# Kernel optimization log

Measured on AMD Instinct MI355X. Metric: run time of the kernel, lower is better.

The kernel has to match this reference:

```python
import jax, jax.numpy as jnp
import numpy as np
from jax.scipy.special import logsumexp

K, V, D, R, S_ITERS = 512, 50257, 300, 75, 20


def setup_inputs() -> dict:
    key = jax.random.key(0)
    ks = jax.random.split(key, 4)
    word_embeds = jax.random.normal(ks[0], (V, D), dtype=jnp.float32)  # frozen GloVe table
    anchors = jax.random.normal(ks[1], (K, D), dtype=jnp.float32) * 0.02
    M_U = jax.random.normal(ks[2], (D, R), dtype=jnp.float32) * (1.0 / D ** 0.5)
    # word_proj initialized to identity in torch (nn.init.eye_); add tiny noise to avoid degeneracy
    Wp = jnp.eye(D, dtype=jnp.float32) + 0.01 * jax.random.normal(ks[3], (D, D), dtype=jnp.float32)
    log_eps = jnp.float32(-2.3)
    topic_scale = jnp.ones((K, 1), dtype=jnp.float32)
    return {"word_embeds": word_embeds, "anchors": anchors, "M_U": M_U,
            "Wp": Wp, "log_eps": log_eps, "topic_scale": topic_scale}


def _l2norm(x):
    # F.normalize(dim=-1) with eps clamp
    n = jnp.maximum(jnp.linalg.norm(x, axis=-1, keepdims=True), 1e-12)
    return x / n


def reference(word_embeds, anchors, M_U, Wp, log_eps, topic_scale):
    # torch Linear: x @ W.T
    w = _l2norm(word_embeds @ Wp.T)   # [V, d]
    a = _l2norm(anchors)              # [K, d]

    # Mahalanobis cost with M = I + U U^T
    M = jnp.eye(D, dtype=w.dtype) + M_U @ M_U.T    # [d, d]
    MA = a @ M                                      # [K, d]
    MW = w @ M                                      # [V, d]
    AA = jnp.sum(MA * a, axis=-1)                   # [K]
    WW = jnp.sum(MW * w, axis=-1)                   # [V]
    cost = jnp.maximum(AA[:, None] + WW[None, :] - 2.0 * (MA @ w.T), 0.0)  # [K, V]

    eps = jax.nn.softplus(log_eps) + 1e-4
    log_kern = -cost / eps                          # [K, V]

    # 20-step log-domain Sinkhorn
    def body(carry, _):
        log_u, log_v = carry
        log_u = -logsumexp(log_kern + log_v, axis=1, keepdims=True)  # [K, 1]
        log_v = -logsumexp(log_kern + log_u, axis=0, keepdims=True)  # [1, V]
        return (log_u, log_v), None

    init = (jnp.zeros((K, 1), log_kern.dtype), jnp.zeros((1, V), log_kern.dtype))
    (log_u, log_v), _ = jax.lax.scan(body, init, None, length=S_ITERS)

    log_P = log_kern + log_u + log_v
    log_beta = log_P - logsumexp(log_P, axis=1, keepdims=True)
    beta = jnp.exp(log_beta) * jax.nn.softplus(topic_scale)
    beta = beta / jnp.sum(beta, axis=1, keepdims=True)
    return beta  # [K, V]
```

## Files before the change

### kernel.cpp

```cpp
#include <hip/hip_runtime.h>
#include <math.h>

#define KT 512
#define VW 50257
#define DD 300
#define RR 75
#define DR 375
#define GAMMA 0.010187536f
#define NB 786
#define SLOTS 8

typedef _Float16 half8 __attribute__((ext_vector_type(8)));
typedef float f32x4 __attribute__((ext_vector_type(4)));

__device__ __forceinline__ void load_lds16(const void* g, void* l) {
  __builtin_amdgcn_global_load_lds(
      (const __attribute__((address_space(1))) unsigned int*)g,
      (__attribute__((address_space(3))) unsigned int*)l, 16, 0, 0);
}

__device__ inline float block_reduce_sum(float val, float* sbuf) {
  int t = threadIdx.x;
  sbuf[t] = val;
  __syncthreads();
  for (int off = blockDim.x >> 1; off > 0; off >>= 1) {
    if (t < off) sbuf[t] += sbuf[t + off];
    __syncthreads();
  }
  float r = sbuf[0];
  __syncthreads();
  return r;
}

template <int CTRL>
__device__ __forceinline__ float dpp_add_step(float x) {
  int yi = __builtin_amdgcn_update_dpp(0, __float_as_int(x), CTRL, 0xf, 0xf, false);
  return x + __int_as_float(yi);
}
__device__ __forceinline__ float wave_reduce_add(float x) {
  x = dpp_add_step<0x111>(x);
  x = dpp_add_step<0x112>(x);
  x = dpp_add_step<0x114>(x);
  x = dpp_add_step<0x118>(x);
  x = dpp_add_step<0x142>(x);
  x = dpp_add_step<0x143>(x);
  return x;
}

__global__ void prep_We_split(const float* __restrict__ We, _Float16* __restrict__ We2) {
  int v = blockIdx.x, c = threadIdx.x;
  float x = (c < DD) ? We[(size_t)v * DD + c] : 0.f;
  _Float16 h = (_Float16)x;
  We2[(size_t)v * 640 + c] = h;
  We2[(size_t)v * 640 + 320 + c] = (_Float16)(x - (float)h);
}

__global__ void prep_bext(const float* __restrict__ Wp, const float* __restrict__ MU,
                          float* __restrict__ Bext) {
  int id = blockIdx.x * blockDim.x + threadIdx.x;
  if (id >= DR * DD) return;
  int row = id / DD, d = id - row * DD;
  if (row < DD) {
    Bext[id] = Wp[row * DD + d];
  } else {
    int r = row - DD;
    float s = 0.f;
    for (int j = 0; j < DD; ++j) s += MU[j * RR + r] * Wp[j * DD + d];
    Bext[id] = s;
  }
}

__global__ void prep_bext_split(const float* __restrict__ BextR, _Float16* __restrict__ Bext2) {
  int r = blockIdx.x, c = threadIdx.x;
  float x = (r < DR && c < DD) ? BextR[r * DD + c] : 0.f;
  _Float16 h = (_Float16)x;
  Bext2[(size_t)r * 640 + c] = h;
  Bext2[(size_t)r * 640 + 320 + c] = (_Float16)(x - (float)h);
}

__global__ void prep_anchors(const float* __restrict__ anchors, const float* __restrict__ MU,
                             _Float16* __restrict__ Ahat2, float* __restrict__ AA) {
  __shared__ float a[DD];
  __shared__ float psh[RR];
  __shared__ float red[128];
  __shared__ float inv_sh;
  int k = blockIdx.x, t = threadIdx.x;
  float ss = 0.f;
  for (int d = t; d < DD; d += 128) {
    float x = anchors[k * DD + d];
    a[d] = x;
    ss += x * x;
  }
  ss = block_reduce_sum(ss, red);
  if (t == 0) inv_sh = 1.f / fmaxf(sqrtf(ss), 1e-12f);
  __syncthreads();
  float inv = inv_sh;
  float p2 = 0.f;
  if (t < RR) {
    float p = 0.f;
    for (int j = 0; j < DD; ++j) p += MU[j * RR + t] * a[j];
    p *= inv;
    psh[t] = p;
    p2 = p * p;
  }
  p2 = block_reduce_sum(p2, red);
  _Float16* row = Ahat2 + (size_t)k * 768;
  for (int d = t; d < 384; d += 128) {
    float val = (d < DD) ? a[d] * inv : ((d < DR) ? psh[d - DD] : 0.f);
    _Float16 h = (_Float16)val;
    row[d] = h;
    row[384 + d] = (_Float16)(val - (float)h);
  }
  if (t == 0) AA[k] = 1.f + p2;
}

__global__ void prep_words(float* __restrict__ WhatR, float* __restrict__ WW) {
  __shared__ float red[128];
  __shared__ float inv_sh;
  int v = blockIdx.x, t = threadIdx.x;
  float* rowf = WhatR + (size_t)v * 384;
  float x0 = rowf[t];
  float x1 = rowf[t + 128];
  float x2 = (t + 256 < DR) ? rowf[t + 256] : 0.f;
  float ss = x0 * x0 + x1 * x1 + ((t < 44) ? x2 * x2 : 0.f);
  ss = block_reduce_sum(ss, red);
  if (t == 0) inv_sh = 1.f / fmaxf(sqrtf(ss), 1e-12f);
  __syncthreads();
  float inv = inv_sh;
  x0 *= inv; x1 *= inv; x2 *= inv;
  float p2 = (t >= 44 && t + 256 < DR) ? x2 * x2 : 0.f;
  p2 = block_reduce_sum(p2, red);
  _Float16* rowh = (_Float16*)rowf;
  _Float16 h0 = (_Float16)x0;
  rowh[t] = h0; rowh[384 + t] = (_Float16)(x0 - (float)h0);
  _Float16 h1 = (_Float16)x1;
  rowh[128 + t] = h1; rowh[512 + t] = (_Float16)(x1 - (float)h1);
  float v2 = (t + 256 < DR) ? x2 : 0.f;
  _Float16 h2 = (_Float16)v2;
  rowh[256 + t] = h2; rowh[640 + t] = (_Float16)(v2 - (float)h2);
  if (t == 0) WW[v] = 1.f + p2;
}

template <int EPI>
__global__ __launch_bounds__(256) void gemm_mfma(
    const _Float16* __restrict__ Ag, int ldaE,
    const _Float16* __restrict__ Bg, int ldbE,
    float* __restrict__ C, long ldc,
    int M, int N, int KTOT, int SEGL, int mOnX,
    const float* __restrict__ AAv, const float* __restrict__ WWv,
    const float* __restrict__ log_eps_ptr) {
  __shared__ __align__(16) _Float16 As[128 * 64];
  __shared__ __align__(16) _Float16 Bs[128 * 64];
  int t = threadIdx.x, lane = t & 63, w = t >> 6;

  int nwg = gridDim.x * gridDim.y;
  int orig = blockIdx.y * gridDim.x + blockIdx.x;
  int q = nwg >> 3, r8 = nwg & 7;
  int xcd = orig & 7, pos = orig >> 3;
  int wgid = (xcd < r8 ? xcd * (q + 1) : r8 * (q + 1) + (xcd - r8) * q) + pos;
  int bxi = wgid % gridDim.x;
  int byi = wgid / gridDim.x;

  int bm = (mOnX ? bxi : byi) * 128;
  int bn = (mOnX ? byi : bxi) * 128;
  int wm = w >> 1, wn = w & 1;
  f32x4 acc[4][4] = {};
  size_t ldaB = (size_t)ldaE * 2, ldbB = (size_t)ldbE * 2;
  int srow = lane >> 3, sg = lane & 7;
  int lr = lane & 15, kq = lane >> 4;

  for (int k0 = 0; k0 < KTOT; k0 += 64) {
    int ak = (k0 >= 2 * SEGL) ? k0 - 2 * SEGL : k0;
    int bk = (k0 >= SEGL) ? k0 - SEGL : k0;
    size_t akb = (size_t)ak * 2, bkb = (size_t)bk * 2;
#pragma unroll
    for (int qq = 0; qq < 4; ++qq) {
      int iid = w * 4 + qq;
      int r = iid * 8 + srow;
      int gs = sg ^ (r & 7);
      int gmr = bm + r; if (gmr >= M) gmr = M - 1;
      load_lds16((const char*)Ag + (size_t)gmr * ldaB + akb + (gs << 4),
                 (char*)As + iid * 1024);
      int gnr = bn + r; if (gnr >= N) gnr = N - 1;
      load_lds16((const char*)Bg + (size_t)gnr * ldbB + bkb + (gs << 4),
                 (char*)Bs + iid * 1024);
    }
    __syncthreads();
#pragma unroll
    for (int ks = 0; ks < 2; ++ks) {
      half8 af[4], bf[4];
#pragma unroll
      for (int i = 0; i < 4; ++i) {
        int row = wm * 64 + i * 16 + lr;
        af[i] = *(const half8*)((const char*)As + row * 128 +
                                ((((ks << 2) + kq) ^ (row & 7)) << 4));
        int col = wn * 64 + i * 16 + lr;
        bf[i] = *(const half8*)((const char*)Bs + col * 128 +
                                ((((ks << 2) + kq) ^ (col & 7)) << 4));
      }
#pragma unroll
      for (int i = 0; i < 4; ++i)
#pragma unroll
        for (int j = 0; j < 4; ++j)
          acc[i][j] = __builtin_amdgcn_mfma_f32_16x16x32_f16(af[i], bf[j], acc[i][j], 0, 0, 0);
    }
    __syncthreads();
  }

  float s2e = 0.f;
  if (EPI == 1) {
    float le = log_eps_ptr[0];
    float eps = log1pf(__expf(le)) + 1e-4f;
    s2e = 1.4426950408889634f / eps;
  }
  int rq = lane >> 4;
#pragma unroll
  for (int i = 0; i < 4; ++i) {
#pragma unroll
    for (int j = 0; j < 4; ++j) {
#pragma unroll
      for (int r = 0; r < 4; ++r) {
        int gm = bm + wm * 64 + i * 16 + rq * 4 + r;
        int gn = bn + wn * 64 + j * 16 + lr;
        if (gm < M && gn < N) {
          float c = acc[i][j][r];
          if (EPI == 0) {
            C[(size_t)gm * ldc + gn] = c;
          } else {
            float e = exp2f((2.f * c - AAv[gm] - WWv[gn]) * s2e);
            C[(size_t)gm * ldc + gn] = fminf(e, 1.0f);
          }
        }
      }
    }
  }
}

template <int FIRST>
__global__ __launch_bounds__(512) void sweep(const float* __restrict__ E,
                                             const float* __restrict__ Sprev,
                                             float* __restrict__ Scur,
                                             float* __restrict__ vout) {
  __shared__ float u_sh[KT];
  __shared__ float colp[8][64];
  __shared__ float v_sh[64];
  __shared__ float rowacc[KT];
  int t = threadIdx.x;
  int c1 = t & 63, kr = t >> 6;
  int c0 = blockIdx.x * 64;
  int col = c0 + c1;
  bool valid = col < VW;

  if (!FIRST) {
    float s = 0.f;
#pragma unroll
    for (int q = 0; q < SLOTS; ++q) s += Sprev[q * KT + t];
    u_sh[t] = 1.0f / fmaxf(s, 1e-35f);
    __syncthreads();
  }

  float tile[64];
  const float* p = E + (size_t)kr * VW + col;
#pragma unroll
  for (int j = 0; j < 64; ++j) {
    tile[j] = valid ? *p : 0.f;
    p += (size_t)8 * VW;
  }

  float v;
  if (FIRST) {
    v = 1.0f;
  } else {
    float cs = 0.f;
#pragma unroll
    for (int j = 0; j < 64; ++j) cs = fmaf(tile[j], u_sh[kr + 8 * j], cs);
    colp[kr][c1] = cs;
    __syncthreads();
    if (t < 64) {
      float s = 0.f;
#pragma unroll
      for (int q = 0; q < 8; ++q) s += colp[q][t];
      float vv = (c0 + t < VW) ? GAMMA / fmaxf(s, 1e-35f) : 0.f;
      v_sh[t] = vv;
      if (c0 + t < VW) vout[c0 + t] = vv;
    }
    __syncthreads();
    v = v_sh[c1];
  }

#pragma unroll
  for (int j = 0; j < 64; ++j) {
    float x = wave_reduce_add(tile[j] * v);
    if (c1 == 63) rowacc[kr + 8 * j] = x;
  }
  __syncthreads();
  unsafeAtomicAdd(&Scur[(blockIdx.x & (SLOTS - 1)) * KT + t], rowacc[t]);
}

__global__ __launch_bounds__(256) void write_beta(float* __restrict__ out,
                                                  const float* __restrict__ Sfin,
                                                  const float* __restrict__ vv) {
  __shared__ float uk_sh;
  int k = blockIdx.y;
  int t = threadIdx.x;
  if (t == 0) {
    float s = 0.f;
#pragma unroll
    for (int q = 0; q < SLOTS; ++q) s += Sfin[q * KT + k];
    uk_sh = 1.0f / fmaxf(s, 1e-35f);
  }
  __syncthreads();
  float uk = uk_sh;
  int v = blockIdx.x * 256 + t;
  if (v >= VW) return;
  size_t id = (size_t)k * VW + v;
  out[id] = out[id] * (uk * vv[v]);
}

extern "C" void kernel_launch(void* const* d_in, const int* in_sizes, int n_in,
                              void* d_out, int out_size, void* d_ws, size_t ws_size,
                              hipStream_t stream) {
  const float* We = (const float*)d_in[0];
  const float* An = (const float*)d_in[1];
  const float* MU = (const float*)d_in[2];
  const float* Wp = (const float*)d_in[3];
  const float* log_eps = (const float*)d_in[4];
  float* out = (float*)d_out;

  char* p = (char*)d_ws;
  auto take = [&](size_t b) { char* r = p; p += (b + 255) & ~(size_t)255; return r; };
  _Float16* We2   = (_Float16*)take((size_t)VW * 640 * 2);
  _Float16* Bext2 = (_Float16*)take((size_t)384 * 640 * 2);
  _Float16* Ahat2 = (_Float16*)take((size_t)KT * 768 * 2);
  float* WhatR    = (float*)take((size_t)VW * 384 * 4);
  float* BextR    = (float*)take((size_t)DR * DD * 4);
  float* AA       = (float*)take(KT * 4);
  float* WW       = (float*)take((size_t)VW * 4);
  float* Sbuf     = (float*)take((size_t)21 * SLOTS * KT * 4);
  float* VVb      = (float*)take((size_t)VW * 4);
  _Float16* What2 = (_Float16*)WhatR;

  (void)hipMemsetAsync(Sbuf, 0, (size_t)21 * SLOTS * KT * 4, stream);

  prep_We_split<<<VW, 320, 0, stream>>>(We, We2);
  prep_bext<<<(DR * DD + 255) / 256, 256, 0, stream>>>(Wp, MU, BextR);
  prep_bext_split<<<384, 320, 0, stream>>>(BextR, Bext2);
  prep_anchors<<<KT, 128, 0, stream>>>(An, MU, Ahat2, AA);

  gemm_mfma<0><<<dim3(3, 393), 256, 0, stream>>>(
      We2, 640, Bext2, 640, WhatR, 384, VW, 384, 960, 320, 0,
      nullptr, nullptr, nullptr);

  prep_words<<<VW, 128, 0, stream>>>(WhatR, WW);

  gemm_mfma<1><<<dim3(4, 393), 256, 0, stream>>>(
      Ahat2, 768, What2, 768, out, VW, KT, VW, 1152, 384, 1,
      AA, WW, log_eps);

  sweep<1><<<NB, 512, 0, stream>>>(out, nullptr, Sbuf, nullptr);
  for (int s = 1; s <= 20; ++s) {
    sweep<0><<<NB, 512, 0, stream>>>(out, Sbuf + (size_t)(s - 1) * SLOTS * KT,
                                     Sbuf + (size_t)s * SLOTS * KT, VVb);
  }

  dim3 g3((VW + 255) / 256, KT);
  write_beta<<<g3, 256, 0, stream>>>(out, Sbuf + (size_t)20 * SLOTS * KT, VVb);
}
```

Measured before the change: 940.2 us.

## Fuse Sinkhorn iterations into one cooperative kernel with register-resident tiles

Replaces 21 separate sweep launches and the write_beta pass with a single cooperative kernel. Each of 252 blocks of 1024 threads keeps its slice of the 512x50257 kernel matrix in registers across all iterations, using grid syncs between iterations. This removes the repeated re-reading of the ~100MB matrix from global memory each iteration and the final read-modify-write pass. In exchange it needs 100 floats of registers per thread and enough residency for all blocks at once. It also depends on grid-wide sync cost and a reduced parallel footprint.

```diff
diff --git a/kernel.cpp b/kernel.cpp
--- a/kernel.cpp
+++ b/kernel.cpp
@@ -1,5 +1,8 @@
 #include <hip/hip_runtime.h>
+#include <hip/hip_cooperative_groups.h>
 #include <math.h>
+
+namespace cg = cooperative_groups;
 
 #define KT 512
 #define VW 50257
@@ -7,8 +10,8 @@
 #define RR 75
 #define DR 375
 #define GAMMA 0.010187536f
-#define NB 786
 #define SLOTS 8
+#define CB 252
 
 typedef _Float16 half8 __attribute__((ext_vector_type(8)));
 typedef float f32x4 __attribute__((ext_vector_type(4)));
@@ -236,85 +239,94 @@
   }
 }
 
-template <int FIRST>
-__global__ __launch_bounds__(512) void sweep(const float* __restrict__ E,
-                                             const float* __restrict__ Sprev,
-                                             float* __restrict__ Scur,
-                                             float* __restrict__ vout) {
-  __shared__ float u_sh[KT];
-  __shared__ float colp[8][64];
-  __shared__ float v_sh[64];
-  __shared__ float rowacc[KT];
+__global__ __launch_bounds__(1024, 4) void coop_sinkhorn(float* __restrict__ EB,
+                                                         float* __restrict__ Sbuf) {
+  cg::grid_group gg = cg::this_grid();
+  __shared__ float colp[16][100];
+  __shared__ float v_sh[200];
+  __shared__ float rowp[512][2];
   int t = threadIdx.x;
-  int c1 = t & 63, kr = t >> 6;
-  int c0 = blockIdx.x * 64;
-  int col = c0 + c1;
-  bool valid = col < VW;
-
-  if (!FIRST) {
+  int h = t >> 9, r = t & 511, w = t >> 6;
+  int cbase = blockIdx.x * 200 + h * 100;
+  float* base = EB + (size_t)r * VW + cbase;
+  int slot = blockIdx.x & (SLOTS - 1);
+  bool full = (cbase + 100 <= VW);
+
+  float tile[100];
+  if (full) {
+#pragma unroll
+    for (int j = 0; j < 100; ++j) tile[j] = base[j];
+  } else {
+#pragma unroll
+    for (int j = 0; j < 100; ++j) tile[j] = (cbase + j < VW) ? base[j] : 0.f;
+  }
+
+  {
+    float rs = 0.f;
+#pragma unroll
+    for (int j = 0; j < 100; ++j) rs += tile[j];
+    rowp[r][h] = rs;
+    __syncthreads();
+    if (t < 512)
+      unsafeAtomicAdd(&Sbuf[(size_t)slot * KT + t], rowp[t][0] + rowp[t][1]);
+    gg.sync();
+  }
+
+  for (int it = 1; it <= 20; ++it) {
+    const float* Sp = Sbuf + (size_t)(it - 1) * SLOTS * KT;
     float s = 0.f;
 #pragma unroll
-    for (int q = 0; q < SLOTS; ++q) s += Sprev[q * KT + t];
-    u_sh[t] = 1.0f / fmaxf(s, 1e-35f);
-    __syncthreads();
-  }
-
-  float tile[64];
-  const float* p = E + (size_t)kr * VW + col;
-#pragma unroll
-  for (int j = 0; j < 64; ++j) {
-    tile[j] = valid ? *p : 0.f;
-    p += (size_t)8 * VW;
-  }
-
-  float v;
-  if (FIRST) {
-    v = 1.0f;
-  } else {
-    float cs = 0.f;
-#pragma unroll
-    for (int j = 0; j < 64; ++j) cs = fmaf(tile[j], u_sh[kr + 8 * j], cs);
-    colp[kr][c1] = cs;
-    __syncthreads();
-    if (t < 64) {
-      float s = 0.f;
-#pragma unroll
-      for (int q = 0; q < 8; ++q) s += colp[q][t];
-      float vv = (c0 + t < VW) ? GAMMA / fmaxf(s, 1e-35f) : 0.f;
-      v_sh[t] = vv;
-      if (c0 + t < VW) vout[c0 + t] = vv;
-    }
-    __syncthreads();
-    v = v_sh[c1];
-  }
-
-#pragma unroll
-  for (int j = 0; j < 64; ++j) {
-    float x = wave_reduce_add(tile[j] * v);
-    if (c1 == 63) rowacc[kr + 8 * j] = x;
-  }
-  __syncthreads();
-  unsafeAtomicAdd(&Scur[(blockIdx.x & (SLOTS - 1)) * KT + t], rowacc[t]);
-}
-
-__global__ __launch_bounds__(256) void write_beta(float* __restrict__ out,
-                                                  const float* __restrict__ Sfin,
-                                                  const float* __restrict__ vv) {
-  __shared__ float uk_sh;
-  int k = blockIdx.y;
-  int t = threadIdx.x;
-  if (t == 0) {
+    for (int q = 0; q < SLOTS; ++q) s += Sp[q * KT + r];
+    float u = 1.0f / fmaxf(s, 1e-35f);
+
+#pragma unroll
+    for (int j = 0; j < 100; ++j) {
+      float x = wave_reduce_add(tile[j] * u);
+      if ((t & 63) == 63) colp[w][j] = x;
+    }
+    __syncthreads();
+    if (t < 200) {
+      int half = t / 100, jj = t - half * 100;
+      float cs = 0.f;
+#pragma unroll
+      for (int q = 0; q < 8; ++q) cs += colp[half * 8 + q][jj];
+      v_sh[t] = GAMMA / fmaxf(cs, 1e-35f);
+    }
+    __syncthreads();
+
+    const float4* vv4 = (const float4*)&v_sh[h * 100];
+    float rs = 0.f;
+#pragma unroll
+    for (int j4 = 0; j4 < 25; ++j4) {
+      float4 v4 = vv4[j4];
+      rs = fmaf(tile[j4 * 4 + 0], v4.x, rs);
+      rs = fmaf(tile[j4 * 4 + 1], v4.y, rs);
+      rs = fmaf(tile[j4 * 4 + 2], v4.z, rs);
+      rs = fmaf(tile[j4 * 4 + 3], v4.w, rs);
+    }
+    rowp[r][h] = rs;
+    __syncthreads();
+    if (t < 512)
+      unsafeAtomicAdd(&Sbuf[(size_t)it * SLOTS * KT + slot * KT + t],
+                      rowp[t][0] + rowp[t][1]);
+    gg.sync();
+  }
+
+  {
+    const float* Sp = Sbuf + (size_t)20 * SLOTS * KT;
     float s = 0.f;
 #pragma unroll
-    for (int q = 0; q < SLOTS; ++q) s += Sfin[q * KT + k];
-    uk_sh = 1.0f / fmaxf(s, 1e-35f);
-  }
-  __syncthreads();
-  float uk = uk_sh;
-  int v = blockIdx.x * 256 + t;
-  if (v >= VW) return;
-  size_t id = (size_t)k * VW + v;
-  out[id] = out[id] * (uk * vv[v]);
+    for (int q = 0; q < SLOTS; ++q) s += Sp[q * KT + r];
+    float up = 1.0f / fmaxf(s, 1e-35f);
+    if (full) {
+#pragma unroll
+      for (int j = 0; j < 100; ++j) base[j] = tile[j] * (up * v_sh[h * 100 + j]);
+    } else {
+#pragma unroll
+      for (int j = 0; j < 100; ++j)
+        if (cbase + j < VW) base[j] = tile[j] * (up * v_sh[h * 100 + j]);
+    }
+  }
 }
 
 extern "C" void kernel_launch(void* const* d_in, const int* in_sizes, int n_in,
@@ -337,7 +349,6 @@
   float* AA       = (float*)take(KT * 4);
   float* WW       = (float*)take((size_t)VW * 4);
   float* Sbuf     = (float*)take((size_t)21 * SLOTS * KT * 4);
-  float* VVb      = (float*)take((size_t)VW * 4);
   _Float16* What2 = (_Float16*)WhatR;
 
   (void)hipMemsetAsync(Sbuf, 0, (size_t)21 * SLOTS * KT * 4, stream);
@@ -357,12 +368,7 @@
       Ahat2, 768, What2, 768, out, VW, KT, VW, 1152, 384, 1,
       AA, WW, log_eps);
 
-  sweep<1><<<NB, 512, 0, stream>>>(out, nullptr, Sbuf, nullptr);
-  for (int s = 1; s <= 20; ++s) {
-    sweep<0><<<NB, 512, 0, stream>>>(out, Sbuf + (size_t)(s - 1) * SLOTS * KT,
-                                     Sbuf + (size_t)s * SLOTS * KT, VVb);
-  }
-
-  dim3 g3((VW + 255) / 256, KT);
-  write_beta<<<g3, 256, 0, stream>>>(out, Sbuf + (size_t)20 * SLOTS * KT, VVb);
-}
+  void* kargs[] = {(void*)&out, (void*)&Sbuf};
+  (void)hipLaunchCooperativeKernel((void*)coop_sinkhorn, dim3(CB), dim3(1024),
+                                   kargs, 0, stream);
+}
```

After: 1.111 ms. 18.2% more time.

## Vectorize Sinkhorn sweep loads, double-buffer GEMM LDS, vectorize beta write

Applied to the files above, without the earlier changes.

Double-buffers the GEMM shared-memory tiles so the next K-slice's global-to-LDS loads are issued while MFMAs run on the current one. The sinkhorn sweep kernel is restructured so each thread reads float4 chunks across 4 columns for 32 row groups, instead of scalar per-column loads. This reduces per-lane DPP reduction depth to 16 lanes and widens memory transactions. write_beta also switches to float4 unaligned vector accesses, with a scalar tail path. The cost is doubled LDS use in the GEMM (possible occupancy loss) and unaligned f4 loads, since the VW row stride is odd.

```diff
diff --git a/kernel.cpp b/kernel.cpp
--- a/kernel.cpp
+++ b/kernel.cpp
@@ -12,6 +12,7 @@
 
 typedef _Float16 half8 __attribute__((ext_vector_type(8)));
 typedef float f32x4 __attribute__((ext_vector_type(4)));
+typedef float f4a __attribute__((ext_vector_type(4), aligned(4)));
 
 __device__ __forceinline__ void load_lds16(const void* g, void* l) {
   __builtin_amdgcn_global_load_lds(
@@ -37,13 +38,11 @@
   int yi = __builtin_amdgcn_update_dpp(0, __float_as_int(x), CTRL, 0xf, 0xf, false);
   return x + __int_as_float(yi);
 }
-__device__ __forceinline__ float wave_reduce_add(float x) {
+__device__ __forceinline__ float row16_reduce_add(float x) {
   x = dpp_add_step<0x111>(x);
   x = dpp_add_step<0x112>(x);
   x = dpp_add_step<0x114>(x);
   x = dpp_add_step<0x118>(x);
-  x = dpp_add_step<0x142>(x);
-  x = dpp_add_step<0x143>(x);
   return x;
 }
 
@@ -149,8 +148,8 @@
     int M, int N, int KTOT, int SEGL, int mOnX,
     const float* __restrict__ AAv, const float* __restrict__ WWv,
     const float* __restrict__ log_eps_ptr) {
-  __shared__ __align__(16) _Float16 As[128 * 64];
-  __shared__ __align__(16) _Float16 Bs[128 * 64];
+  __shared__ __align__(16) _Float16 As[2 * 128 * 64];
+  __shared__ __align__(16) _Float16 Bs[2 * 128 * 64];
   int t = threadIdx.x, lane = t & 63, w = t >> 6;
 
   int nwg = gridDim.x * gridDim.y;
@@ -168,8 +167,10 @@
   size_t ldaB = (size_t)ldaE * 2, ldbB = (size_t)ldbE * 2;
   int srow = lane >> 3, sg = lane & 7;
   int lr = lane & 15, kq = lane >> 4;
-
-  for (int k0 = 0; k0 < KTOT; k0 += 64) {
+  int NT = KTOT >> 6;
+
+  auto stage = [&](int buf, int kt) {
+    int k0 = kt << 6;
     int ak = (k0 >= 2 * SEGL) ? k0 - 2 * SEGL : k0;
     int bk = (k0 >= SEGL) ? k0 - SEGL : k0;
     size_t akb = (size_t)ak * 2, bkb = (size_t)bk * 2;
@@ -180,22 +181,30 @@
       int gs = sg ^ (r & 7);
       int gmr = bm + r; if (gmr >= M) gmr = M - 1;
       load_lds16((const char*)Ag + (size_t)gmr * ldaB + akb + (gs << 4),
-                 (char*)As + iid * 1024);
+                 (char*)As + buf * 16384 + iid * 1024);
       int gnr = bn + r; if (gnr >= N) gnr = N - 1;
       load_lds16((const char*)Bg + (size_t)gnr * ldbB + bkb + (gs << 4),
-                 (char*)Bs + iid * 1024);
-    }
-    __syncthreads();
+                 (char*)Bs + buf * 16384 + iid * 1024);
+    }
+  };
+
+  stage(0, 0);
+  __syncthreads();
+  int cur = 0;
+  for (int kt = 0; kt < NT; ++kt) {
+    if (kt + 1 < NT) stage(cur ^ 1, kt + 1);
+    const char* Ab = (const char*)As + cur * 16384;
+    const char* Bb = (const char*)Bs + cur * 16384;
 #pragma unroll
     for (int ks = 0; ks < 2; ++ks) {
       half8 af[4], bf[4];
 #pragma unroll
       for (int i = 0; i < 4; ++i) {
         int row = wm * 64 + i * 16 + lr;
-        af[i] = *(const half8*)((const char*)As + row * 128 +
+        af[i] = *(const half8*)(Ab + row * 128 +
                                 ((((ks << 2) + kq) ^ (row & 7)) << 4));
         int col = wn * 64 + i * 16 + lr;
-        bf[i] = *(const half8*)((const char*)Bs + col * 128 +
+        bf[i] = *(const half8*)(Bb + col * 128 +
                                 ((((ks << 2) + kq) ^ (col & 7)) << 4));
       }
 #pragma unroll
@@ -205,6 +214,7 @@
           acc[i][j] = __builtin_amdgcn_mfma_f32_16x16x32_f16(af[i], bf[j], acc[i][j], 0, 0, 0);
     }
     __syncthreads();
+    cur ^= 1;
   }
 
   float s2e = 0.f;
@@ -242,59 +252,78 @@
                                              float* __restrict__ Scur,
                                              float* __restrict__ vout) {
   __shared__ float u_sh[KT];
-  __shared__ float colp[8][64];
-  __shared__ float v_sh[64];
+  __shared__ __align__(16) float colp[32][64];
+  __shared__ __align__(16) float v_sh[64];
   __shared__ float rowacc[KT];
   int t = threadIdx.x;
-  int c1 = t & 63, kr = t >> 6;
+  int c4 = t & 15, rg = t >> 4;
   int c0 = blockIdx.x * 64;
-  int col = c0 + c1;
-  bool valid = col < VW;
-
-  if (!FIRST) {
+  int colb = c0 + c4 * 4;
+  bool full = (c0 + 64 <= VW);
+
+  float4 tl[16];
+  const float* bp = E + (size_t)rg * VW + colb;
+  if (full) {
+#pragma unroll
+    for (int j = 0; j < 16; ++j) {
+      f4a x = *(const f4a*)bp;
+      tl[j] = make_float4(x.x, x.y, x.z, x.w);
+      bp += (size_t)32 * VW;
+    }
+  } else {
+#pragma unroll
+    for (int j = 0; j < 16; ++j) {
+      float4 x;
+      x.x = (colb + 0 < VW) ? bp[0] : 0.f;
+      x.y = (colb + 1 < VW) ? bp[1] : 0.f;
+      x.z = (colb + 2 < VW) ? bp[2] : 0.f;
+      x.w = (colb + 3 < VW) ? bp[3] : 0.f;
+      tl[j] = x;
+      bp += (size_t)32 * VW;
+    }
+  }
+
+  float4 vq;
+  if (FIRST) {
+    vq = make_float4(1.f, 1.f, 1.f, 1.f);
+  } else {
     float s = 0.f;
 #pragma unroll
     for (int q = 0; q < SLOTS; ++q) s += Sprev[q * KT + t];
     u_sh[t] = 1.0f / fmaxf(s, 1e-35f);
     __syncthreads();
-  }
-
-  float tile[64];
-  const float* p = E + (size_t)kr * VW + col;
-#pragma unroll
-  for (int j = 0; j < 64; ++j) {
-    tile[j] = valid ? *p : 0.f;
-    p += (size_t)8 * VW;
-  }
-
-  float v;
-  if (FIRST) {
-    v = 1.0f;
-  } else {
-    float cs = 0.f;
-#pragma unroll
-    for (int j = 0; j < 64; ++j) cs = fmaf(tile[j], u_sh[kr + 8 * j], cs);
-    colp[kr][c1] = cs;
+    float4 cs = make_float4(0.f, 0.f, 0.f, 0.f);
+#pragma unroll
+    for (int j = 0; j < 16; ++j) {
+      float u = u_sh[rg + 32 * j];
+      cs.x = fmaf(tl[j].x, u, cs.x);
+      cs.y = fmaf(tl[j].y, u, cs.y);
+      cs.z = fmaf(tl[j].z, u, cs.z);
+      cs.w = fmaf(tl[j].w, u, cs.w);
+    }
+    *(float4*)&colp[rg][c4 * 4] = cs;
     __syncthreads();
     if (t < 64) {
-      float s = 0.f;
-#pragma unroll
-      for (int q = 0; q < 8; ++q) s += colp[q][t];
-      float vv = (c0 + t < VW) ? GAMMA / fmaxf(s, 1e-35f) : 0.f;
+      float s2 = 0.f;
+#pragma unroll
+      for (int q = 0; q < 32; ++q) s2 += colp[q][t];
+      float vv = (c0 + t < VW) ? GAMMA / fmaxf(s2, 1e-35f) : 0.f;
       v_sh[t] = vv;
       if (c0 + t < VW) vout[c0 + t] = vv;
     }
     __syncthreads();
-    v = v_sh[c1];
-  }
-
-#pragma unroll
-  for (int j = 0; j < 64; ++j) {
-    float x = wave_reduce_add(tile[j] * v);
-    if (c1 == 63) rowacc[kr + 8 * j] = x;
-  }
-  __syncthreads();
-  unsafeAtomicAdd(&Scur[(blockIdx.x & (SLOTS - 1)) * KT + t], rowacc[t]);
+    vq = *(const float4*)&v_sh[c4 * 4];
+  }
+
+#pragma unroll
+  for (int j = 0; j < 16; ++j) {
+    float x = fmaf(tl[j].x, vq.x, fmaf(tl[j].y, vq.y,
+              fmaf(tl[j].z, vq.z, tl[j].w * vq.w)));
+    x = row16_reduce_add(x);
+    if (c4 == 15) rowacc[rg + 32 * j] = x;
+  }
+  __syncthreads();
+  unsafeAtomicAdd(&Scur[(size_t)(blockIdx.x & (SLOTS - 1)) * KT + t], rowacc[t]);
 }
 
 __global__ __launch_bounds__(256) void write_beta(float* __restrict__ out,
@@ -311,10 +340,24 @@
   }
   __syncthreads();
   float uk = uk_sh;
-  int v = blockIdx.x * 256 + t;
-  if (v >= VW) return;
-  size_t id = (size_t)k * VW + v;
-  out[id] = out[id] * (uk * vv[v]);
+  int v4 = (blockIdx.x * 256 + t) * 4;
+  if (v4 + 4 <= VW) {
+    size_t id = (size_t)k * VW + v4;
+    f4a e = *(const f4a*)(out + id);
+    float4 w = *(const float4*)(vv + v4);
+    f4a o;
+    o.x = e.x * (uk * w.x); o.y = e.y * (uk * w.y);
+    o.z = e.z * (uk * w.z); o.w = e.w * (uk * w.w);
+    *(f4a*)(out + id) = o;
+  } else {
+#pragma unroll
+    for (int j = 0; j < 4; ++j) {
+      if (v4 + j < VW) {
+        size_t id = (size_t)k * VW + v4 + j;
+        out[id] = out[id] * (uk * vv[v4 + j]);
+      }
+    }
+  }
 }
 
 extern "C" void kernel_launch(void* const* d_in, const int* in_sizes, int n_in,
@@ -363,6 +406,6 @@
                                      Sbuf + (size_t)s * SLOTS * KT, VVb);
   }
 
-  dim3 g3((VW + 255) / 256, KT);
+  dim3 g3((VW + 1023) / 1024, KT);
   write_beta<<<g3, 256, 0, stream>>>(out, Sbuf + (size_t)20 * SLOTS * KT, VVb);
 }
```

Result: faster. 862.3 us (-8.3%).
